# Performance work log

Hardware: AMD Instinct MI355X
Metric: run time of the kernel (lower is better)

The kernel has to match this reference:

```python
import jax, jax.numpy as jnp
import numpy as np

NUM_CLASSES = 64
NUM_HEADS = 12


def setup_inputs() -> dict:
    key = jax.random.key(0)
    k1, k2, k3 = jax.random.split(key, 3)
    rel_pos = jax.random.randint(k1, (4, 2048, 2048), 0, NUM_CLASSES, dtype=jnp.int64 if jax.config.jax_enable_x64 else jnp.int32)
    hidden_states = jax.random.normal(k2, (4, 2048, 16), dtype=jnp.float32)
    # nn.Linear(64, 12, bias=False) weight: [out_features=12, in_features=64]
    W = jax.random.normal(k3, (NUM_HEADS, NUM_CLASSES), dtype=jnp.float32) * (1.0 / np.sqrt(NUM_CLASSES))
    return {"rel_pos": rel_pos, "hidden_states": hidden_states, "W": W}


def reference(rel_pos, hidden_states, W):
    # one_hot(rel_pos, 64).type_as(hidden) @ W.T  ==  gather rows of W.T at rel_pos
    table = W.T.astype(hidden_states.dtype)          # [64, 12]
    return jnp.take(table, rel_pos, axis=0)          # [B, S, S, 12]
```

## Files before the change

kernel.cpp:

```cpp
#include <hip/hip_runtime.h>
#include <hip/hip_bf16.h>

#define BLOCK 256

__global__ __launch_bounds__(BLOCK) void gather12_kernel(
    const int* __restrict__ rel_pos,
    const float* __restrict__ W,
    float4* __restrict__ out,
    unsigned int total_chunks)
{
    __shared__ float tab[64 * 12];

    const int t = threadIdx.x;
    for (int i = t; i < 768; i += BLOCK) {
        int h = i >> 6;
        int c = i & 63;
        tab[c * 12 + h] = W[i];
    }
    __syncthreads();

    const unsigned int stride = gridDim.x * BLOCK;
    for (unsigned int q = blockIdx.x * BLOCK + t; q < total_chunks; q += stride) {
        unsigned int p = q / 3u;
        unsigned int s = q - p * 3u;
        unsigned int c = (unsigned int)rel_pos[p];
        const float4 v = *(const float4*)(tab + c * 12u + 4u * s);
        out[q] = v;
    }
}

extern "C" void kernel_launch(void* const* d_in, const int* in_sizes, int n_in,
                              void* d_out, int out_size, void* d_ws, size_t ws_size,
                              hipStream_t stream)
{
    const int* rel_pos = (const int*)d_in[0];
    const float* W = (const float*)d_in[2];

    const long long n_rec = in_sizes[0];
    const unsigned int total_chunks = (unsigned int)(n_rec * 3ll);

    const int iters = 8;
    long long threads_needed = ((long long)total_chunks + iters - 1) / iters;
    int blocks = (int)((threads_needed + BLOCK - 1) / BLOCK);
    if (blocks < 1) blocks = 1;

    gather12_kernel<<<blocks, BLOCK, 0, stream>>>(rel_pos, W, (float4*)d_out, total_chunks);
}
```

Baseline: 878.4 us.

## Stage class indices in LDS per block and write output with nontemporal stores

Result: faster. 830.4 us (-5.5%).

```diff
diff --git a/kernel.cpp b/kernel.cpp
--- a/kernel.cpp
+++ b/kernel.cpp
@@ -3,13 +3,16 @@
 
 #define BLOCK 256
 
-__global__ __launch_bounds__(BLOCK) void gather12_kernel(
+typedef float f4 __attribute__((ext_vector_type(4)));
+
+__global__ __launch_bounds__(BLOCK) void gather12_v3(
     const int* __restrict__ rel_pos,
     const float* __restrict__ W,
-    float4* __restrict__ out,
-    unsigned int total_chunks)
+    f4* __restrict__ out,
+    unsigned int n_rec)
 {
     __shared__ float tab[64 * 12];
+    __shared__ int cls[BLOCK];
 
     const int t = threadIdx.x;
     for (int i = t; i < 768; i += BLOCK) {
@@ -17,15 +20,29 @@
         int c = i & 63;
         tab[c * 12 + h] = W[i];
     }
+
+    const unsigned int recBase = blockIdx.x * BLOCK;
+    const unsigned int r = recBase + t;
+    cls[t] = (r < n_rec) ? rel_pos[r] : 0;
     __syncthreads();
 
-    const unsigned int stride = gridDim.x * BLOCK;
-    for (unsigned int q = blockIdx.x * BLOCK + t; q < total_chunks; q += stride) {
-        unsigned int p = q / 3u;
-        unsigned int s = q - p * 3u;
-        unsigned int c = (unsigned int)rel_pos[p];
-        const float4 v = *(const float4*)(tab + c * 12u + 4u * s);
-        out[q] = v;
+    const unsigned long long chunkBase = (unsigned long long)recBase * 3ull;
+    const unsigned long long total_chunks = (unsigned long long)n_rec * 3ull;
+
+    f4 v[3];
+#pragma unroll
+    for (int k = 0; k < 3; ++k) {
+        unsigned int j = (unsigned int)t + BLOCK * k;
+        unsigned int p = j / 3u;
+        unsigned int s = j - p * 3u;
+        unsigned int c = (unsigned int)cls[p];
+        v[k] = *(const f4*)(tab + c * 12u + 4u * s);
+    }
+#pragma unroll
+    for (int k = 0; k < 3; ++k) {
+        unsigned int j = (unsigned int)t + BLOCK * k;
+        if (chunkBase + j < total_chunks)
+            __builtin_nontemporal_store(v[k], &out[chunkBase + j]);
     }
 }
 
@@ -36,13 +53,8 @@
     const int* rel_pos = (const int*)d_in[0];
     const float* W = (const float*)d_in[2];
 
-    const long long n_rec = in_sizes[0];
-    const unsigned int total_chunks = (unsigned int)(n_rec * 3ll);
+    const unsigned int n_rec = (unsigned int)in_sizes[0];
+    const int blocks = (int)((n_rec + BLOCK - 1) / BLOCK);
 
-    const int iters = 8;
-    long long threads_needed = ((long long)total_chunks + iters - 1) / iters;
-    int blocks = (int)((threads_needed + BLOCK - 1) / BLOCK);
-    if (blocks < 1) blocks = 1;
-
-    gather12_kernel<<<blocks, BLOCK, 0, stream>>>(rel_pos, W, (float4*)d_out, total_chunks);
+    gather12_v3<<<blocks, BLOCK, 0, stream>>>(rel_pos, W, (f4*)d_out, n_rec);
 }
```
